# Kernel tuning notes

Hardware: AMD Instinct MI355X
Metric: run time of the kernel (lower is better)

Reference implementation:

```python
import jax, jax.numpy as jnp
import numpy as np
import math

H = 16          # num_attention_heads
D = 1024        # hidden_size
DH = D // H     # size_per_head = 64


def setup_inputs() -> dict:
    key = jax.random.key(0)
    ks = jax.random.split(key, 8)
    B, S = 4, 2048
    std = 0.02
    inputs = jax.random.normal(ks[0], (B, S, D), dtype=jnp.float32)
    attention_mask = jax.random.randint(ks[1], (B, S), 0, 2, dtype=jnp.int32)
    Wq = jax.random.normal(ks[2], (D, D), dtype=jnp.float32) * std
    Wk = jax.random.normal(ks[3], (D, D), dtype=jnp.float32) * std
    Wv = jax.random.normal(ks[4], (D, D), dtype=jnp.float32) * std
    bq = jnp.zeros((D,), dtype=jnp.float32)
    bk = jnp.zeros((D,), dtype=jnp.float32)
    bv = jnp.zeros((D,), dtype=jnp.float32)
    return {"inputs": inputs, "attention_mask": attention_mask,
            "Wq": Wq, "bq": bq, "Wk": Wk, "bk": bk, "Wv": Wv, "bv": bv}


def reference(inputs, attention_mask, Wq, bq, Wk, bk, Wv, bv):
    B, S, _ = inputs.shape
    scale = 1.0 / math.sqrt(float(DH))

    def split_heads(x):  # [B,S,D] -> [B,H,S,DH]
        return x.reshape(B, S, H, DH).transpose(0, 2, 1, 3)

    q = split_heads(inputs @ Wq + bq)
    k = split_heads(inputs @ Wk + bk)
    v = split_heads(inputs @ Wv + bv)

    # [B,H,S,S] scores
    scores = jnp.einsum('bhqd,bhkd->bhqk', q, k) * scale
    # additive mask: (1 - mask[b, k]) * -10000, broadcast over heads and query pos
    mask = attention_mask.astype(jnp.float32)[:, None, None, :]  # [B,1,1,S]
    scores = scores + (1.0 - mask) * -10000.0

    probs = jax.nn.softmax(scores, axis=-1)  # dropout prob = 0.0 -> identity
    out = jnp.einsum('bhqk,bhkd->bhqd', probs, v)  # [B,H,S,DH]
    return out.transpose(0, 2, 1, 3).reshape(B, S, D)
```

## Files before the change

kernel.cpp:

```cpp
#include <hip/hip_runtime.h>
#include <cstddef>

#define NH 16
#define DMODEL 1024
#define DHD 64
#define BB 4
#define SS 2048
#define MROWS (BB * SS)
#define XE ((size_t)MROWS * DMODEL)

typedef __attribute__((ext_vector_type(8))) short short8;
typedef __attribute__((ext_vector_type(4))) short short4v;
typedef __attribute__((ext_vector_type(4))) float f32x4;
typedef __attribute__((ext_vector_type(16))) float f32x16;
typedef __attribute__((ext_vector_type(4))) int i32x4;

__device__ __forceinline__ float bf2f(unsigned short u) {
    return __uint_as_float(((unsigned int)u) << 16);
}
__device__ __forceinline__ unsigned short f2bf(float f) {
    unsigned int u = __float_as_uint(f);
    u += 0x7fffu + ((u >> 16) & 1u);
    return (unsigned short)(u >> 16);
}

__device__ __forceinline__ int detect_f32(const unsigned short* X, int tid,
                                          int* flagShared) {
    if (tid < 64) {
        unsigned e = (X[2 * tid] >> 7) & 0xFFu;
        unsigned long long m = __ballot(e >= 100u && e <= 150u);
        if (tid == 0) *flagShared = (__popcll(m) < 48) ? 1 : 0;
    }
    __syncthreads();
    return *flagShared;
}

__device__ __forceinline__ void gl2lds16(const unsigned short* g,
                                         unsigned short* l) {
    __builtin_amdgcn_global_load_lds(
        (const __attribute__((address_space(1))) unsigned int*)g,
        (__attribute__((address_space(3))) unsigned int*)l, 16, 0, 0);
}

__global__ __launch_bounds__(256) void conv_x(
    const unsigned short* __restrict__ X, unsigned short* __restrict__ Scr)
{
    __shared__ int dflag;
    int isf32 = detect_f32(X, threadIdx.x, &dflag);
    if (!isf32) return;
    const float* Xf = (const float*)X;
    size_t i0 = ((size_t)blockIdx.x * 256 + threadIdx.x) * 8;
    f32x4 a = *(const f32x4*)(Xf + i0);
    f32x4 b = *(const f32x4*)(Xf + i0 + 4);
    short8 o;
#pragma unroll
    for (int j = 0; j < 4; j++) { o[j] = (short)f2bf(a[j]); o[4 + j] = (short)f2bf(b[j]); }
    *(short8*)(Scr + i0) = o;
}

__global__ __launch_bounds__(256) void conv_w(
    const unsigned short* __restrict__ Wq,
    const unsigned short* __restrict__ Wk,
    const unsigned short* __restrict__ Wv,
    const unsigned short* __restrict__ Xdet,
    unsigned short* __restrict__ Scr)
{
    __shared__ float tile[64][65];
    __shared__ int dflag;
    int isf32 = detect_f32(Xdet, threadIdx.x, &dflag);
    unsigned short* Wt = Scr + (isf32 ? XE : 0);
    int mat = blockIdx.z;
    const unsigned short* Ws = (mat == 0) ? Wq : ((mat == 1) ? Wk : Wv);
    const float* Wf = (const float*)Ws;
    int n0 = blockIdx.x * 64, k0 = blockIdx.y * 64;
    int tx = threadIdx.x & 63, ty = threadIdx.x >> 6;
#pragma unroll
    for (int p = 0; p < 16; p++) {
        int k = ty + 4 * p;
        float v = isf32 ? Wf[(size_t)(k0 + k) * DMODEL + n0 + tx]
                        : bf2f(Ws[(size_t)(k0 + k) * DMODEL + n0 + tx]);
        tile[k][tx] = v;
    }
    __syncthreads();
    unsigned short* Wm = Wt + (size_t)mat * DMODEL * DMODEL;
#pragma unroll
    for (int p = 0; p < 16; p++) {
        int n = ty + 4 * p;
        Wm[(size_t)(n0 + n) * DMODEL + k0 + tx] = f2bf(tile[tx][n]);
    }
}

__global__ __launch_bounds__(256, 3) void qkv_gemm(
    const unsigned short* __restrict__ Xorig,
    const unsigned short* __restrict__ Scr,
    const unsigned short* __restrict__ bq,
    const unsigned short* __restrict__ bk,
    const unsigned short* __restrict__ bv,
    unsigned short* __restrict__ Q,
    unsigned short* __restrict__ K,
    unsigned short* __restrict__ Vt)
{
    __shared__ __align__(16) unsigned short arena[17408];
    __shared__ int dflag;
#define AS_(r) (&arena[(size_t)(r) * 64])
#define BS_(r) (&arena[8192 + (size_t)(r) * 64])

    int tid = threadIdx.x, lane = tid & 63, w = tid >> 6;
    int wr = w >> 1, wc = w & 1, quad = lane >> 4, c = lane & 15;
    int m0 = blockIdx.x * 128;
    int by = blockIdx.y;
    int mat = by >> 3;
    int nb = (by & 7) * 128;

    int isf32 = detect_f32(Xorig, tid, &dflag);
    const unsigned short* Xsrc = isf32 ? Scr : Xorig;
    const unsigned short* Wt = Scr + (isf32 ? XE : 0);
    const unsigned short* Wrows = Wt + ((size_t)mat * DMODEL + nb) * DMODEL;

    int srow = lane >> 3;
    int scol = (lane & 7) * 8;

    f32x4 acc[4][4];
#pragma unroll
    for (int a = 0; a < 4; a++)
#pragma unroll
        for (int b2 = 0; b2 < 4; b2++) acc[a][b2] = (f32x4){0.f, 0.f, 0.f, 0.f};

    for (int k0 = 0; k0 < DMODEL; k0 += 64) {
        __syncthreads();
#pragma unroll
        for (int t = 0; t < 4; t++) {
            int r = w * 32 + t * 8 + srow;
            gl2lds16(Xsrc + (size_t)(m0 + r) * DMODEL + k0 + scol,
                     AS_(w * 32 + t * 8));
            gl2lds16(Wrows + (size_t)r * DMODEL + k0 + scol,
                     BS_(w * 32 + t * 8));
        }
        __syncthreads();

#pragma unroll
        for (int ks = 0; ks < 2; ks++) {
            short8 af[4], bf[4];
#pragma unroll
            for (int t = 0; t < 4; t++) {
                af[t] = *(const short8*)(AS_(wr * 64 + t * 16 + c) + ks * 32 + quad * 8);
                bf[t] = *(const short8*)(BS_(wc * 64 + t * 16 + c) + ks * 32 + quad * 8);
            }
#pragma unroll
            for (int rt = 0; rt < 4; rt++)
#pragma unroll
                for (int ct = 0; ct < 4; ct++)
                    acc[rt][ct] = __builtin_amdgcn_mfma_f32_16x16x32_bf16(
                        af[rt], bf[ct], acc[rt][ct], 0, 0, 0);
        }
    }

    const unsigned short* bias = (mat == 0) ? bq : ((mat == 1) ? bk : bv);
    float qscale = (mat == 0) ? 0.18033688f : 1.0f;

    if (mat == 2) {
        __syncthreads();
#pragma unroll
        for (int ct = 0; ct < 4; ct++) {
            int nloc = wc * 64 + ct * 16 + c;
            int nl = nb + nloc;
            float bvv = isf32 ? ((const float*)bias)[nl] : bf2f(bias[nl]);
#pragma unroll
            for (int rt = 0; rt < 4; rt++) {
                int sloc = wr * 64 + rt * 16 + quad * 4;
                short4v pk;
#pragma unroll
                for (int i = 0; i < 4; i++)
                    pk[i] = (short)f2bf(acc[rt][ct][i] + bvv);
                *(short4v*)&arena[(size_t)nloc * 136 + sloc] = pk;
            }
        }
        __syncthreads();
        int b_ = m0 >> 11, s0_ = m0 & 2047;
#pragma unroll
        for (int it = 0; it < 8; it++) {
            int idx = it * 256 + tid;
            int nloc = idx >> 4, sc = idx & 15;
            int ncol = nb + nloc;
            int hl2 = ncol >> 6, dd = ncol & 63;
            short8 vv = *(const short8*)&arena[(size_t)nloc * 136 + sc * 8];
            *(short8*)(Vt + ((size_t)(b_ * NH + hl2) * DHD + dd) * SS +
                       s0_ + sc * 8) = vv;
        }
    } else {
#pragma unroll
        for (int ct = 0; ct < 4; ct++) {
            int nl = nb + wc * 64 + ct * 16 + c;
            float bvv = isf32 ? ((const float*)bias)[nl] : bf2f(bias[nl]);
            int hl = nl >> 6, d = nl & 63;
#pragma unroll
            for (int rt = 0; rt < 4; rt++) {
                int r0 = m0 + wr * 64 + rt * 16 + quad * 4;
                int b_ = r0 >> 11, s_ = r0 & 2047;
                int bh = b_ * NH + hl;
                unsigned short* dst =
                    ((mat == 0) ? Q : K) + ((size_t)bh * SS + s_) * DHD + d;
#pragma unroll
                for (int i = 0; i < 4; i++)
                    dst[(size_t)i * DHD] = f2bf((acc[rt][ct][i] + bvv) * qscale);
            }
        }
    }
#undef AS_
#undef BS_
}


#define STAGE(B_, kb_)                                                       \
    {                                                                        \
        int kbv = (kb_);                                                     \
        gl2lds16(Kh + (size_t)(kbv + l31) * DHD + (2 * w + hi) * 8,          \
                 &KT[B_][w * 512]);                                          \
        gl2lds16(Vth + (size_t)lane * SS + kbv + w * 8,                      \
                 &VT[B_][w * 512]);                                          \
    }

#define MVLOAD(mv_, kb_)                                                     \
    {                                                                        \
        int kbv = (kb_);                                                     \
        _Pragma("unroll")                                                    \
        for (int g = 0; g < 4; g++)                                          \
            mv_[g] = *(const i32x4*)(maskb + kbv + 8 * g + 4 * hi);          \
    }

#define COMPUTESTEP(B_, mv_)                                                 \
    {                                                                        \
        short8 kf[4];                                                        \
        _Pragma("unroll")                                                    \
        for (int d = 0; d < 4; d++)                                          \
            kf[d] = *(const short8*)&KT[B_][(2 * d + hi) * 256 + l31 * 8];   \
        short8 vf[2][2];                                                     \
        _Pragma("unroll")                                                    \
        for (int dt = 0; dt < 2; dt++)                                       \
            _Pragma("unroll")                                                \
            for (int kt = 0; kt < 2; kt++)                                   \
                vf[dt][kt] = *(const short8*)&VT[B_][(2 * kt + hi) * 512 +   \
                                                     dt * 256 + l31 * 8];    \
        _Pragma("unroll")                                                    \
        for (int qq = 0; qq < 2; qq++) {                                     \
            f32x16 s;                                                        \
            _Pragma("unroll")                                                \
            for (int r = 0; r < 16; r++)                                     \
                s[r] = mv_[r >> 2][r & 3] ? 0.0f : -16384.0f;                \
            _Pragma("unroll")                                                \
            for (int d = 0; d < 4; d++)                                      \
                s = __builtin_amdgcn_mfma_f32_32x32x16_bf16(kf[d], qf[qq][d],\
                                                            s, 0, 0, 0);     \
            float p[16];                                                     \
            float ps0 = 0.f, ps1 = 0.f;                                      \
            _Pragma("unroll")                                                \
            for (int r = 0; r < 16; r++) {                                   \
                float pv = __builtin_amdgcn_exp2f(s[r]);                     \
                p[r] = pv;                                                   \
                if (r & 1) ps1 += pv; else ps0 += pv;                        \
            }                                                                \
            psum[qq] += ps0 + ps1;                                           \
            int aw[8];                                                       \
            _Pragma("unroll")                                                \
            for (int t = 0; t < 8; t++)                                      \
                asm("v_cvt_pk_bf16_f32 %0, %1, %2"                           \
                    : "=v"(aw[t]) : "v"(p[2 * t]), "v"(p[2 * t + 1]));       \
            asm("v_permlane32_swap_b32 %0, %1" : "+v"(aw[0]), "+v"(aw[2]));  \
            asm("v_permlane32_swap_b32 %0, %1" : "+v"(aw[1]), "+v"(aw[3]));  \
            asm("v_permlane32_swap_b32 %0, %1" : "+v"(aw[4]), "+v"(aw[6]));  \
            asm("v_permlane32_swap_b32 %0, %1" : "+v"(aw[5]), "+v"(aw[7]));  \
            i32x4 f0 = {aw[0], aw[1], aw[2], aw[3]};                         \
            i32x4 f1 = {aw[4], aw[5], aw[6], aw[7]};                         \
            short8 pf0 = __builtin_bit_cast(short8, f0);                     \
            short8 pf1 = __builtin_bit_cast(short8, f1);                     \
            _Pragma("unroll")                                                \
            for (int dt = 0; dt < 2; dt++) {                                 \
                oacc[dt][qq] = __builtin_amdgcn_mfma_f32_32x32x16_bf16(      \
                    vf[dt][0], pf0, oacc[dt][qq], 0, 0, 0);                  \
                oacc[dt][qq] = __builtin_amdgcn_mfma_f32_32x32x16_bf16(      \
                    vf[dt][1], pf1, oacc[dt][qq], 0, 0, 0);                  \
            }                                                                \
        }                                                                    \
    }

__global__ __launch_bounds__(256, 2) void attn(
    const unsigned short* __restrict__ Q,
    const unsigned short* __restrict__ Kg,
    const unsigned short* __restrict__ Vt,
    const int* __restrict__ mask,
    unsigned short* __restrict__ OutBase,
    const unsigned short* __restrict__ Xdet)
{
    __shared__ __align__(16) unsigned short KT[2][2048];
    __shared__ __align__(16) unsigned short VT[2][2048];

    int tid = threadIdx.x;
    int lane = tid & 63, w = tid >> 6;
    int l31 = lane & 31, hi = lane >> 5;

    unsigned ex = ((unsigned)Xdet[2 * lane] >> 7) & 0xFFu;
    unsigned long long bm = __ballot(ex >= 100u && ex <= 150u);
    int isf32 = (__popcll(bm) < 48) ? 1 : 0;

    int lin = blockIdx.x;
    int bh = (lin & 7) + (((lin >> 3) & 7) << 3);
    int qt = lin >> 6;
    int bz = bh >> 4, hl = bh & 15;

    const unsigned short* Qh = Q + (size_t)bh * SS * DHD;
    const unsigned short* Kh = Kg + (size_t)bh * SS * DHD;
    const unsigned short* Vth = Vt + (size_t)bh * DHD * SS;
    const int* maskb = mask + (size_t)bz * SS;

    int q0 = qt * 256 + w * 64;

    short8 qf[2][4];
#pragma unroll
    for (int qq = 0; qq < 2; qq++)
#pragma unroll
        for (int d = 0; d < 4; d++)
            qf[qq][d] = *(const short8*)(Qh + (size_t)(q0 + qq * 32 + l31) * DHD +
                                         d * 16 + hi * 8);

    f32x16 oacc[2][2];
    float psum[2] = {0.f, 0.f};
#pragma unroll
    for (int dt = 0; dt < 2; dt++)
#pragma unroll
        for (int qq = 0; qq < 2; qq++)
#pragma unroll
            for (int r = 0; r < 16; r++) oacc[dt][qq][r] = 0.f;

    i32x4 mvA[4], mvB[4];

    STAGE(0, 0);
    MVLOAD(mvA, 0);
    __syncthreads();

    for (int kb = 0; kb < SS; kb += 64) {
        STAGE(1, kb + 32);
        MVLOAD(mvB, kb + 32);
        COMPUTESTEP(0, mvA);
        __syncthreads();

        if (kb + 64 < SS) {
            STAGE(0, kb + 64);
            MVLOAD(mvA, kb + 64);
        }
        COMPUTESTEP(1, mvB);
        __syncthreads();
    }

    long obase = (long)bz * SS * DMODEL;
    unsigned short* Outh = OutBase + obase;
    float* Outf = (float*)OutBase + obase;
#pragma unroll
    for (int qq = 0; qq < 2; qq++) {
        float tot = psum[qq] + __shfl_xor(psum[qq], 32);
        float inv = 1.0f / tot;
        int q = q0 + qq * 32 + l31;
#pragma unroll
    for (int dt = 0; dt < 2; dt++) {
#pragma unroll
            for (int g = 0; g < 4; g++) {
                int dbase = dt * 32 + 8 * g + 4 * hi;
                size_t base = (size_t)q * DMODEL + hl * DHD + dbase;
                if (isf32) {
                    f32x4 ov;
#pragma unroll
                    for (int j = 0; j < 4; j++)
                        ov[j] = oacc[dt][qq][4 * g + j] * inv;
                    *(f32x4*)(Outf + base) = ov;
                } else {
                    short4v ov;
#pragma unroll
                    for (int j = 0; j < 4; j++)
                        ov[j] = (short)f2bf(oacc[dt][qq][4 * g + j] * inv);
                    *(short4v*)(Outh + base) = ov;
                }
            }
        }
    }
}

extern "C" void kernel_launch(void* const* d_in, const int* in_sizes, int n_in,
                              void* d_out, int out_size, void* d_ws, size_t ws_size,
                              hipStream_t stream)
{
    const unsigned short* X    = (const unsigned short*)d_in[0];
    const int*            mask = (const int*)d_in[1];
    const unsigned short* Wq   = (const unsigned short*)d_in[2];
    const unsigned short* bq   = (const unsigned short*)d_in[3];
    const unsigned short* Wk   = (const unsigned short*)d_in[4];
    const unsigned short* bk   = (const unsigned short*)d_in[5];
    const unsigned short* Wv   = (const unsigned short*)d_in[6];
    const unsigned short* bv   = (const unsigned short*)d_in[7];

    unsigned short* Scr = (unsigned short*)d_out;

    unsigned short* Qw  = (unsigned short*)d_ws;
    unsigned short* Kw  = Qw + (size_t)BB * NH * SS * DHD;
    unsigned short* Vtw = Kw + (size_t)BB * NH * SS * DHD;

    conv_x<<<dim3((unsigned)(XE / (256 * 8))), 256, 0, stream>>>(X, Scr);
    conv_w<<<dim3(16, 16, 3), 256, 0, stream>>>(Wq, Wk, Wv, X, Scr);
    qkv_gemm<<<dim3(64, 24), 256, 0, stream>>>(
        X, Scr, bq, bk, bv, Qw, Kw, Vtw);
    attn<<<dim3(512), 256, 0, stream>>>(
        Qw, Kw, Vtw, mask, (unsigned short*)d_out, X);
}
```

Before: 250.7 us.

## Halve per-wave query tile in attention to raise occupancy and block count

Each wave now handles 32 query rows instead of 64, so a block covers 128 queries and the grid doubles to 1024 blocks. Register use for accumulators and Q fragments halves, and launch bounds go from 2 to 3 blocks per CU. The aim is more resident waves to hide latency. In exchange, K/V tiles staged in shared memory are reused across half as many queries, doubling K/V global traffic and LDS reads per unit of work.

```diff
diff --git a/kernel.cpp b/kernel.cpp
--- a/kernel.cpp
+++ b/kernel.cpp
@@ -241,49 +241,46 @@
             for (int kt = 0; kt < 2; kt++)                                   \
                 vf[dt][kt] = *(const short8*)&VT[B_][(2 * kt + hi) * 512 +   \
                                                      dt * 256 + l31 * 8];    \
-        _Pragma("unroll")                                                    \
-        for (int qq = 0; qq < 2; qq++) {                                     \
-            f32x16 s;                                                        \
-            _Pragma("unroll")                                                \
-            for (int r = 0; r < 16; r++)                                     \
-                s[r] = mv_[r >> 2][r & 3] ? 0.0f : -16384.0f;                \
-            _Pragma("unroll")                                                \
-            for (int d = 0; d < 4; d++)                                      \
-                s = __builtin_amdgcn_mfma_f32_32x32x16_bf16(kf[d], qf[qq][d],\
-                                                            s, 0, 0, 0);     \
-            float p[16];                                                     \
-            float ps0 = 0.f, ps1 = 0.f;                                      \
-            _Pragma("unroll")                                                \
-            for (int r = 0; r < 16; r++) {                                   \
-                float pv = __builtin_amdgcn_exp2f(s[r]);                     \
-                p[r] = pv;                                                   \
-                if (r & 1) ps1 += pv; else ps0 += pv;                        \
-            }                                                                \
-            psum[qq] += ps0 + ps1;                                           \
-            int aw[8];                                                       \
-            _Pragma("unroll")                                                \
-            for (int t = 0; t < 8; t++)                                      \
-                asm("v_cvt_pk_bf16_f32 %0, %1, %2"                           \
-                    : "=v"(aw[t]) : "v"(p[2 * t]), "v"(p[2 * t + 1]));       \
-            asm("v_permlane32_swap_b32 %0, %1" : "+v"(aw[0]), "+v"(aw[2]));  \
-            asm("v_permlane32_swap_b32 %0, %1" : "+v"(aw[1]), "+v"(aw[3]));  \
-            asm("v_permlane32_swap_b32 %0, %1" : "+v"(aw[4]), "+v"(aw[6]));  \
-            asm("v_permlane32_swap_b32 %0, %1" : "+v"(aw[5]), "+v"(aw[7]));  \
-            i32x4 f0 = {aw[0], aw[1], aw[2], aw[3]};                         \
-            i32x4 f1 = {aw[4], aw[5], aw[6], aw[7]};                         \
-            short8 pf0 = __builtin_bit_cast(short8, f0);                     \
-            short8 pf1 = __builtin_bit_cast(short8, f1);                     \
-            _Pragma("unroll")                                                \
-            for (int dt = 0; dt < 2; dt++) {                                 \
-                oacc[dt][qq] = __builtin_amdgcn_mfma_f32_32x32x16_bf16(      \
-                    vf[dt][0], pf0, oacc[dt][qq], 0, 0, 0);                  \
-                oacc[dt][qq] = __builtin_amdgcn_mfma_f32_32x32x16_bf16(      \
-                    vf[dt][1], pf1, oacc[dt][qq], 0, 0, 0);                  \
-            }                                                                \
+        f32x16 s;                                                            \
+        _Pragma("unroll")                                                    \
+        for (int r = 0; r < 16; r++)                                         \
+            s[r] = mv_[r >> 2][r & 3] ? 0.0f : -16384.0f;                    \
+        _Pragma("unroll")                                                    \
+        for (int d = 0; d < 4; d++)                                          \
+            s = __builtin_amdgcn_mfma_f32_32x32x16_bf16(kf[d], qf[d],        \
+                                                        s, 0, 0, 0);         \
+        float p[16];                                                         \
+        float ps0 = 0.f, ps1 = 0.f;                                          \
+        _Pragma("unroll")                                                    \
+        for (int r = 0; r < 16; r++) {                                       \
+            float pv = __builtin_amdgcn_exp2f(s[r]);                         \
+            p[r] = pv;                                                       \
+            if (r & 1) ps1 += pv; else ps0 += pv;                            \
         }                                                                    \
-    }
-
-__global__ __launch_bounds__(256, 2) void attn(
+        psum += ps0 + ps1;                                                   \
+        int aw[8];                                                           \
+        _Pragma("unroll")                                                    \
+        for (int t = 0; t < 8; t++)                                          \
+            asm("v_cvt_pk_bf16_f32 %0, %1, %2"                               \
+                : "=v"(aw[t]) : "v"(p[2 * t]), "v"(p[2 * t + 1]));           \
+        asm("v_permlane32_swap_b32 %0, %1" : "+v"(aw[0]), "+v"(aw[2]));      \
+        asm("v_permlane32_swap_b32 %0, %1" : "+v"(aw[1]), "+v"(aw[3]));      \
+        asm("v_permlane32_swap_b32 %0, %1" : "+v"(aw[4]), "+v"(aw[6]));      \
+        asm("v_permlane32_swap_b32 %0, %1" : "+v"(aw[5]), "+v"(aw[7]));      \
+        i32x4 f0 = {aw[0], aw[1], aw[2], aw[3]};                             \
+        i32x4 f1 = {aw[4], aw[5], aw[6], aw[7]};                             \
+        short8 pf0 = __builtin_bit_cast(short8, f0);                         \
+        short8 pf1 = __builtin_bit_cast(short8, f1);                         \
+        _Pragma("unroll")                                                    \
+        for (int dt = 0; dt < 2; dt++) {                                     \
+            oacc[dt] = __builtin_amdgcn_mfma_f32_32x32x16_bf16(              \
+                vf[dt][0], pf0, oacc[dt], 0, 0, 0);                          \
+            oacc[dt] = __builtin_amdgcn_mfma_f32_32x32x16_bf16(              \
+                vf[dt][1], pf1, oacc[dt], 0, 0, 0);                          \
+        }                                                                    \
+    }
+
+__global__ __launch_bounds__(256, 3) void attn(
     const unsigned short* __restrict__ Q,
     const unsigned short* __restrict__ Kg,
     const unsigned short* __restrict__ Vt,
@@ -312,24 +309,19 @@
     const unsigned short* Vth = Vt + (size_t)bh * DHD * SS;
     const int* maskb = mask + (size_t)bz * SS;
 
-    int q0 = qt * 256 + w * 64;
-
-    short8 qf[2][4];
-#pragma unroll
-    for (int qq = 0; qq < 2; qq++)
-#pragma unroll
-        for (int d = 0; d < 4; d++)
-            qf[qq][d] = *(const short8*)(Qh + (size_t)(q0 + qq * 32 + l31) * DHD +
-                                         d * 16 + hi * 8);
-
-    f32x16 oacc[2][2];
-    float psum[2] = {0.f, 0.f};
+    int q0 = qt * 128 + w * 32;
+
+    short8 qf[4];
+#pragma unroll
+    for (int d = 0; d < 4; d++)
+        qf[d] = *(const short8*)(Qh + (size_t)(q0 + l31) * DHD + d * 16 + hi * 8);
+
+    f32x16 oacc[2];
+    float psum = 0.f;
 #pragma unroll
     for (int dt = 0; dt < 2; dt++)
 #pragma unroll
-        for (int qq = 0; qq < 2; qq++)
-#pragma unroll
-            for (int r = 0; r < 16; r++) oacc[dt][qq][r] = 0.f;
+        for (int r = 0; r < 16; r++) oacc[dt][r] = 0.f;
 
     i32x4 mvA[4], mvB[4];
 
@@ -354,30 +346,27 @@
     long obase = (long)bz * SS * DMODEL;
     unsigned short* Outh = OutBase + obase;
     float* Outf = (float*)OutBase + obase;
-#pragma unroll
-    for (int qq = 0; qq < 2; qq++) {
-        float tot = psum[qq] + __shfl_xor(psum[qq], 32);
-        float inv = 1.0f / tot;
-        int q = q0 + qq * 32 + l31;
+    float tot = psum + __shfl_xor(psum, 32);
+    float inv = 1.0f / tot;
+    int q = q0 + l31;
 #pragma unroll
     for (int dt = 0; dt < 2; dt++) {
 #pragma unroll
-            for (int g = 0; g < 4; g++) {
-                int dbase = dt * 32 + 8 * g + 4 * hi;
-                size_t base = (size_t)q * DMODEL + hl * DHD + dbase;
-                if (isf32) {
-                    f32x4 ov;
-#pragma unroll
-                    for (int j = 0; j < 4; j++)
-                        ov[j] = oacc[dt][qq][4 * g + j] * inv;
-                    *(f32x4*)(Outf + base) = ov;
-                } else {
-                    short4v ov;
-#pragma unroll
-                    for (int j = 0; j < 4; j++)
-                        ov[j] = (short)f2bf(oacc[dt][qq][4 * g + j] * inv);
-                    *(short4v*)(Outh + base) = ov;
-                }
+        for (int g = 0; g < 4; g++) {
+            int dbase = dt * 32 + 8 * g + 4 * hi;
+            size_t base = (size_t)q * DMODEL + hl * DHD + dbase;
+            if (isf32) {
+                f32x4 ov;
+#pragma unroll
+                for (int j = 0; j < 4; j++)
+                    ov[j] = oacc[dt][4 * g + j] * inv;
+                *(f32x4*)(Outf + base) = ov;
+            } else {
+                short4v ov;
+#pragma unroll
+                for (int j = 0; j < 4; j++)
+                    ov[j] = (short)f2bf(oacc[dt][4 * g + j] * inv);
+                *(short4v*)(Outh + base) = ov;
             }
         }
     }
@@ -406,6 +395,6 @@
     conv_w<<<dim3(16, 16, 3), 256, 0, stream>>>(Wq, Wk, Wv, X, Scr);
     qkv_gemm<<<dim3(64, 24), 256, 0, stream>>>(
         X, Scr, bq, bk, bv, Qw, Kw, Vtw);
-    attn<<<dim3(512), 256, 0, stream>>>(
+    attn<<<dim3(1024), 256, 0, stream>>>(
         Qw, Kw, Vtw, mask, (unsigned short*)d_out, X);
 }
```

After: 301.2 us. 20.1% more time.
